# Performance work log

Measured on AMD Instinct MI355X. Metric: run time of the kernel, lower is better.

The kernel has to match this reference:

```python
import jax, jax.numpy as jnp
import numpy as np

EPS = 1e-6
N_HEADS = 16
D_HEAD = 64

def _rmsnorm(x, scale):
    rms = jnp.sqrt(jnp.mean(x * x, axis=-1, keepdims=True) + EPS)
    return x / rms * scale

def setup_inputs() -> dict:
    key = jax.random.key(0)
    ks = jax.random.split(key, 8)
    B, L, D = 512, 64, 1024
    return {
        "x": jax.random.normal(ks[0], (B, L, D), dtype=jnp.float32),
        "rel_indices": jax.random.randint(ks[1], (L, L), 0, 225, dtype=jnp.int64),
        "Wq": jax.random.normal(ks[2], (D, D), dtype=jnp.float32) * 0.02,
        "Wk": jax.random.normal(ks[3], (D, D), dtype=jnp.float32) * 0.02,
        "Wv": jax.random.normal(ks[4], (D, D), dtype=jnp.float32) * 0.02,
        "Wo": jax.random.normal(ks[5], (D, D), dtype=jnp.float32) * 0.02,
        "q_scale": jnp.ones((D_HEAD,), dtype=jnp.float32),
        "k_scale": jnp.ones((D_HEAD,), dtype=jnp.float32),
        "rel_k": jax.random.normal(ks[6], (225, D_HEAD), dtype=jnp.float32) * 0.02,
        "rel_v": jax.random.normal(ks[7], (225, D_HEAD), dtype=jnp.float32) * 0.02,
    }

def reference(x, rel_indices, Wq, Wk, Wv, Wo, q_scale, k_scale, rel_k, rel_v):
    B, L, D = x.shape
    H, dk = N_HEADS, D_HEAD
    scale = 1.0 / jnp.sqrt(jnp.float32(dk))
    # projections; Linear with weight W applied as x @ W (bias=False)
    q = (x @ Wq).reshape(B, L, H, dk)
    k = (x @ Wk).reshape(B, L, H, dk)
    v = (x @ Wv).reshape(B, L, H, dk).transpose(0, 2, 1, 3)  # bhld
    q = _rmsnorm(q, q_scale).transpose(0, 2, 1, 3)  # bhld
    k = _rmsnorm(k, k_scale).transpose(0, 2, 1, 3)  # bhld
    r_k = rel_k[rel_indices]  # [L, L, dk]
    r_v = rel_v[rel_indices]  # [L, L, dk]
    content = jnp.einsum('bhid,bhjd->bhij', q, k)
    rel = jnp.einsum('bhid,ijd->bhij', q, r_k)
    probs = jax.nn.softmax((content + rel) * scale, axis=-1)
    out = jnp.einsum('bhij,bhjd->bhid', probs, v) + jnp.einsum('bhij,ijd->bhid', probs, r_v)
    out = out.transpose(0, 2, 1, 3).reshape(B, L, D)
    return out @ Wo
```

## Files before the change

### kernel.cpp

```cpp
#include <hip/hip_runtime.h>
#include <stdint.h>

typedef unsigned short u16;
typedef __attribute__((ext_vector_type(8))) short s16x8;
typedef __attribute__((ext_vector_type(4))) float f32x4;

#define DEV static __device__ __forceinline__

#define MFMA16(a, b, c) __builtin_amdgcn_mfma_f32_16x16x32_bf16((a), (b), (c), 0, 0, 0)

DEV u16 f2b(float f) {
  unsigned u = __float_as_uint(f);
  unsigned r = (u + 0x7fffu + ((u >> 16) & 1u)) >> 16;
  return (u16)r;
}
DEV float b2f(u16 u) { return __uint_as_float(((unsigned)u) << 16); }

typedef const __attribute__((address_space(1))) unsigned int* as1p;
typedef __attribute__((address_space(3))) unsigned int* as3p;

DEV void gload16(const void* g, void* l) {
  __builtin_amdgcn_global_load_lds((as1p)(uintptr_t)g, (as3p)(unsigned)(uintptr_t)l, 16, 0, 0);
}

DEV void ldsPkAddBf16(void* ldsPtr, unsigned packed) {
  unsigned addr = (unsigned)(uintptr_t)ldsPtr;
  asm volatile("ds_pk_add_bf16 %0, %1" : : "v"(addr), "v"(packed) : "memory");
}

__global__ void conv_x_k(const float* __restrict__ x, u16* __restrict__ xb) {
  const int n8 = 32768 * 1024 / 8;
  int i = blockIdx.x * 256 + threadIdx.x;
  int stride = gridDim.x * 256;
  for (; i < n8; i += stride) {
    const float4* p = (const float4*)x + (size_t)i * 2;
    float4 a = p[0], c = p[1];
    union { s16x8 v; u16 u[8]; } o;
    o.u[0] = f2b(a.x); o.u[1] = f2b(a.y); o.u[2] = f2b(a.z); o.u[3] = f2b(a.w);
    o.u[4] = f2b(c.x); o.u[5] = f2b(c.y); o.u[6] = f2b(c.z); o.u[7] = f2b(c.w);
    *(s16x8*)(xb + (size_t)i * 8) = o.v;
  }
}

__global__ void transp_w_k(const float* __restrict__ Wq, const float* __restrict__ Wk,
                           const float* __restrict__ Wv, const float* __restrict__ Wo,
                           u16* __restrict__ wqkT, u16* __restrict__ wvT, u16* __restrict__ woT) {
  const int z = blockIdx.z;
  const float* src = z == 0 ? Wq : z == 1 ? Wk : z == 2 ? Wv : Wo;
  u16* dst = z == 0 ? wqkT : z == 1 ? (wqkT + 1024 * 1024) : z == 2 ? wvT : woT;
  __shared__ u16 t[64][72];
  const int kb = blockIdx.y * 64, nb = blockIdx.x * 64;
  const int tid = threadIdx.x;
  const int c = tid & 63, r0 = tid >> 6;
  #pragma unroll
  for (int s = 0; s < 16; ++s) {
    int r = r0 * 16 + s;
    t[r][c] = f2b(src[(size_t)(kb + r) * 1024 + nb + c]);
  }
  __syncthreads();
  #pragma unroll
  for (int s = 0; s < 16; ++s) {
    int n = r0 * 16 + s;
    dst[(size_t)(nb + n) * 1024 + kb + c] = t[c][n];
  }
}

__global__ void prep_rel_k(const float* __restrict__ rk, const float* __restrict__ rv,
                           u16* __restrict__ rkb, u16* __restrict__ rvT) {
  int i = blockIdx.x * 256 + threadIdx.x;
  if (i < 240 * 64) {
    int tt = i >> 6, d = i & 63;
    rkb[i] = (tt < 225) ? f2b(rk[tt * 64 + d]) : (u16)0;
  }
  if (i < 64 * 256) {
    int d = i >> 8, tt = i & 255;
    rvT[i] = (tt < 225) ? f2b(rv[tt * 64 + d]) : (u16)0;
  }
}

template <int EPI>
__global__ __launch_bounds__(256, 2)
void gemm_k(const u16* __restrict__ A, const u16* __restrict__ BT,
            u16* __restrict__ o16a, u16* __restrict__ o16b,
            float* __restrict__ oF,
            const float* __restrict__ qsc, const float* __restrict__ ksc) {
  __shared__ u16 smA[2][128 * 32];
  __shared__ u16 smB[2][128 * 32];
  const int tid = threadIdx.x;
  const int w = tid >> 6, l = tid & 63;
  const int lc = l & 15, l4 = l >> 4;
  const int nwg = gridDim.x * gridDim.y;
  const int orig = blockIdx.y * gridDim.x + blockIdx.x;
  const int wg = ((orig & 7) * (nwg >> 3)) + (orig >> 3);
  const int bx = wg % gridDim.x, by = wg / gridDim.x;
  const int m0 = by * 128, n0 = bx * 128;
  const int wm = (w >> 1) * 64, wn = (w & 1) * 64;

  f32x4 acc[4][4];
  #pragma unroll
  for (int i = 0; i < 4; ++i)
    #pragma unroll
    for (int j = 0; j < 4; ++j) acc[i][j] = (f32x4){0.f, 0.f, 0.f, 0.f};

  int srcRow[2], srcCol[2];
  #pragma unroll
  for (int s = 0; s < 2; ++s) {
    int p = w * 2048 + s * 1024 + l * 16;
    int row = p >> 6;
    int lb = p ^ (((row ^ (row >> 2)) & 3) << 4);
    srcRow[s] = row;
    srcCol[s] = (lb & 63) >> 1;
  }

  auto stage = [&](int buf, int kt) {
    #pragma unroll
    for (int s = 0; s < 2; ++s) {
      int base = w * 2048 + s * 1024;
      const u16* ga = A + (size_t)(m0 + srcRow[s]) * 1024 + kt * 32 + srcCol[s];
      gload16(ga, (char*)&smA[buf][0] + base);
      const u16* gb = BT + (size_t)(n0 + srcRow[s]) * 1024 + kt * 32 + srcCol[s];
      gload16(gb, (char*)&smB[buf][0] + base);
    }
  };
  auto fragA = [&](int buf, int mf) -> s16x8 {
    int row = wm + mf * 16 + lc;
    int p = (row << 6) + (l4 << 4);
    p ^= ((row ^ (row >> 2)) & 3) << 4;
    return *(const s16x8*)((const char*)&smA[buf][0] + p);
  };
  auto fragB = [&](int buf, int nf) -> s16x8 {
    int row = wn + nf * 16 + lc;
    int p = (row << 6) + (l4 << 4);
    p ^= ((row ^ (row >> 2)) & 3) << 4;
    return *(const s16x8*)((const char*)&smB[buf][0] + p);
  };

  stage(0, 0);
  __syncthreads();
  #pragma unroll 2
  for (int kt = 0; kt < 32; ++kt) {
    int cur = kt & 1;
    if (kt + 1 < 32) stage(cur ^ 1, kt + 1);
    s16x8 af[4], bf[4];
    #pragma unroll
    for (int i = 0; i < 4; ++i) { af[i] = fragA(cur, i); bf[i] = fragB(cur, i); }
    #pragma unroll
    for (int mf = 0; mf < 4; ++mf)
      #pragma unroll
      for (int nf = 0; nf < 4; ++nf)
        acc[mf][nf] = MFMA16(af[mf], bf[nf], acc[mf][nf]);
    __syncthreads();
  }

  if constexpr (EPI == 2) {
    #pragma unroll
    for (int mf = 0; mf < 4; ++mf)
      #pragma unroll
      for (int r = 0; r < 4; ++r) {
        int gm = m0 + wm + mf * 16 + l4 * 4 + r;
        #pragma unroll
        for (int nf = 0; nf < 4; ++nf) {
          int gn = n0 + wn + nf * 16 + lc;
          oF[(size_t)gm * 1024 + gn] = acc[mf][nf][r];
        }
      }
  } else if constexpr (EPI == 1) {
    #pragma unroll
    for (int mf = 0; mf < 4; ++mf)
      #pragma unroll
      for (int r = 0; r < 4; ++r) {
        int gm = m0 + wm + mf * 16 + l4 * 4 + r;
        #pragma unroll
        for (int nf = 0; nf < 4; ++nf) {
          int gn = n0 + wn + nf * 16 + lc;
          size_t addr = (((size_t)(gn >> 6) * 16 + (gm >> 6)) * 64 + (gm & 63)) * 64 + (gn & 63);
          o16a[addr] = f2b(acc[mf][nf][r]);
        }
      }
  } else {
    int nw0 = n0 + wn;
    bool isq = nw0 < 1024;
    const float* sc = isq ? qsc : ksc;
    u16* dst = isq ? o16a : o16b;
    int h = (nw0 & 1023) >> 6;
    float scv[4];
    #pragma unroll
    for (int nf = 0; nf < 4; ++nf) scv[nf] = sc[nf * 16 + lc];
    #pragma unroll
    for (int mf = 0; mf < 4; ++mf)
      #pragma unroll
      for (int r = 0; r < 4; ++r) {
        float ss = 0.f;
        #pragma unroll
        for (int nf = 0; nf < 4; ++nf) ss += acc[mf][nf][r] * acc[mf][nf][r];
        #pragma unroll
        for (int mask = 1; mask < 16; mask <<= 1) ss += __shfl_xor(ss, mask, 64);
        float rinv = rsqrtf(ss * 0.015625f + 1e-6f);
        int gm = m0 + wm + mf * 16 + l4 * 4 + r;
        size_t base = (((size_t)(gm >> 6) * 16 + h) * 64 + (gm & 63)) * 64;
        #pragma unroll
        for (int nf = 0; nf < 4; ++nf)
          dst[base + nf * 16 + lc] = f2b(acc[mf][nf][r] * rinv * scv[nf]);
      }
  }
}

DEV int rwByte(int row, int t) {
  return row * 512 + ((((t >> 3) ^ (row & 7)) << 4)) + ((t & 7) * 2);
}

__global__ __launch_bounds__(256, 3)
void attn_k(const u16* __restrict__ qn, const u16* __restrict__ kn,
            const u16* __restrict__ vT, const u16* __restrict__ rkb,
            const u16* __restrict__ rvT, const int* __restrict__ ridx,
            u16* __restrict__ ao) {
  __shared__ u16 RW[64 * 256];
  __shared__ u16 Pl[64 * 72];
  const int bid = blockIdx.x;
  const int b = bid >> 4, h = bid & 15;
  const int tid = threadIdx.x;
  const int w = tid >> 6, l = tid & 63;
  const int lc = l & 15, l4 = l >> 4;
  const int i0 = w * 16;
  const size_t hb = (size_t)(b * 16 + h) * 4096;
  const u16* qh = qn + hb;
  const u16* kh = kn + hb;
  const u16* vh = vT + hb;

  int ts[4][4];
  #pragma unroll
  for (int q = 0; q < 4; ++q) {
    int row = i0 + l4 * 4 + q;
    #pragma unroll
    for (int nf = 0; nf < 4; ++nf) ts[nf][q] = ridx[row * 64 + nf * 16 + lc];
  }
  s16x8 aq0 = *(const s16x8*)(qh + (i0 + lc) * 64 + l4 * 8);
  s16x8 aq1 = *(const s16x8*)(qh + (i0 + lc) * 64 + 32 + l4 * 8);
  s16x8 kb0[4], kb1[4], vb0[4], vb1[4];
  #pragma unroll
  for (int nf = 0; nf < 4; ++nf) {
    kb0[nf] = *(const s16x8*)(kh + (nf * 16 + lc) * 64 + l4 * 8);
    kb1[nf] = *(const s16x8*)(kh + (nf * 16 + lc) * 64 + 32 + l4 * 8);
    vb0[nf] = *(const s16x8*)(vh + (nf * 16 + lc) * 64 + l4 * 8);
    vb1[nf] = *(const s16x8*)(vh + (nf * 16 + lc) * 64 + 32 + l4 * 8);
  }

  f32x4 accC[4];
  #pragma unroll
  for (int nf = 0; nf < 4; ++nf) accC[nf] = (f32x4){0.f, 0.f, 0.f, 0.f};
  #pragma unroll
  for (int nf = 0; nf < 4; ++nf) {
    accC[nf] = MFMA16(aq0, kb0[nf], accC[nf]);
    accC[nf] = MFMA16(aq1, kb1[nf], accC[nf]);
  }

  #pragma unroll
  for (int c = 0; c < 3; ++c) {
    s16x8 rb0[5], rb1[5];
    #pragma unroll
    for (int u = 0; u < 5; ++u) {
      int t0 = (c * 5 + u) * 16;
      rb0[u] = *(const s16x8*)(rkb + (t0 + lc) * 64 + l4 * 8);
      rb1[u] = *(const s16x8*)(rkb + (t0 + lc) * 64 + 32 + l4 * 8);
    }
    #pragma unroll
    for (int u = 0; u < 5; ++u) {
      f32x4 rr = (f32x4){0.f, 0.f, 0.f, 0.f};
      rr = MFMA16(aq0, rb0[u], rr);
      rr = MFMA16(aq1, rb1[u], rr);
      int t = (c * 5 + u) * 16 + lc;
      #pragma unroll
      for (int q = 0; q < 4; ++q) {
        int row = i0 + l4 * 4 + q;
        RW[rwByte(row, t) >> 1] = f2b(rr[q]);
      }
    }
  }
  __syncthreads();

  float ev[4][4];
  float linv[4];
  #pragma unroll
  for (int q = 0; q < 4; ++q) {
    int row = i0 + l4 * 4 + q;
    float mx = -1e30f;
    #pragma unroll
    for (int nf = 0; nf < 4; ++nf) {
      float r = b2f(RW[rwByte(row, ts[nf][q]) >> 1]);
      float s = (accC[nf][q] + r) * 0.125f;
      ev[nf][q] = s;
      mx = fmaxf(mx, s);
    }
    #pragma unroll
    for (int mask = 1; mask < 16; mask <<= 1) mx = fmaxf(mx, __shfl_xor(mx, mask, 64));
    float sum = 0.f;
    #pragma unroll
    for (int nf = 0; nf < 4; ++nf) { float e = __expf(ev[nf][q] - mx); ev[nf][q] = e; sum += e; }
    #pragma unroll
    for (int mask = 1; mask < 16; mask <<= 1) sum += __shfl_xor(sum, mask, 64);
    linv[q] = 1.f / sum;
    #pragma unroll
    for (int nf = 0; nf < 4; ++nf) Pl[row * 72 + nf * 16 + lc] = f2b(ev[nf][q]);
  }
  __syncthreads();

  f32x4 accO[4];
  #pragma unroll
  for (int nf = 0; nf < 4; ++nf) accO[nf] = (f32x4){0.f, 0.f, 0.f, 0.f};
  s16x8 pa0 = *(const s16x8*)(&Pl[(i0 + lc) * 72 + l4 * 8]);
  s16x8 pa1 = *(const s16x8*)(&Pl[(i0 + lc) * 72 + 32 + l4 * 8]);
  {
    s16x8 z;
    #pragma unroll
    for (int j = 0; j < 8; ++j) z[j] = 0;
    #pragma unroll
    for (int zz = 0; zz < 8; ++zz) ((s16x8*)RW)[zz * 256 + tid] = z;
  }
  #pragma unroll
  for (int nf = 0; nf < 4; ++nf) {
    accO[nf] = MFMA16(pa0, vb0[nf], accO[nf]);
    accO[nf] = MFMA16(pa1, vb1[nf], accO[nf]);
  }
  __syncthreads();

  #pragma unroll
  for (int q = 0; q < 4; ++q)
    #pragma unroll
    for (int nf = 0; nf < 4; ++nf) {
      int row = i0 + l4 * 4 + q;
      int t = ts[nf][q];
      int byte = row * 512 + ((((t >> 3) ^ (row & 7)) << 4)) + ((t & 6) * 2);
      unsigned pk = ((unsigned)f2b(ev[nf][q])) << ((t & 1) * 16);
      ldsPkAddBf16((char*)RW + byte, pk);
    }
  asm volatile("s_waitcnt lgkmcnt(0)" ::: "memory");
  __syncthreads();

  #pragma unroll
  for (int kc = 0; kc < 4; ++kc) {
    s16x8 rb[2][4], wa[2];
    #pragma unroll
    for (int s = 0; s < 2; ++s) {
      int ks = kc * 2 + s;
      int row = i0 + lc;
      wa[s] = *(const s16x8*)((const char*)RW + row * 512 + ((((ks * 4 + l4) ^ (row & 7))) << 4));
      #pragma unroll
      for (int nf = 0; nf < 4; ++nf)
        rb[s][nf] = *(const s16x8*)(rvT + (nf * 16 + lc) * 256 + ks * 32 + l4 * 8);
    }
    #pragma unroll
    for (int s = 0; s < 2; ++s)
      #pragma unroll
      for (int nf = 0; nf < 4; ++nf)
        accO[nf] = MFMA16(wa[s], rb[s][nf], accO[nf]);
  }

  #pragma unroll
  for (int q = 0; q < 4; ++q) {
    int row = i0 + l4 * 4 + q;
    #pragma unroll
    for (int nf = 0; nf < 4; ++nf) {
      int d = nf * 16 + lc;
      ao[((size_t)(b * 64 + row)) * 1024 + h * 64 + d] = f2b(accO[nf][q] * linv[q]);
    }
  }
}

extern "C" void kernel_launch(void* const* d_in, const int* in_sizes, int n_in,
                              void* d_out, int out_size, void* d_ws, size_t ws_size,
                              hipStream_t stream) {
  (void)in_sizes; (void)n_in; (void)out_size; (void)ws_size;
  const float* x  = (const float*)d_in[0];
  const int* ridx = (const int*)d_in[1];
  const float* Wq = (const float*)d_in[2];
  const float* Wk = (const float*)d_in[3];
  const float* Wv = (const float*)d_in[4];
  const float* Wo = (const float*)d_in[5];
  const float* qs = (const float*)d_in[6];
  const float* ks = (const float*)d_in[7];
  const float* rk = (const float*)d_in[8];
  const float* rv = (const float*)d_in[9];
  float* out = (float*)d_out;

  char* ws = (char*)d_ws;
  const size_t SZ = 32768ull * 1024 * 2;
  u16* xb   = (u16*)(ws);
  u16* qn   = (u16*)(ws + SZ);
  u16* kn   = (u16*)(ws + 2 * SZ);
  u16* vT   = (u16*)(ws + 3 * SZ);
  u16* wqkT = (u16*)(ws + 4 * SZ);
  u16* wvT  = (u16*)(ws + 4 * SZ + 4194304);
  u16* woT  = (u16*)(ws + 4 * SZ + 6291456);
  u16* rkb  = (u16*)(ws + 4 * SZ + 8388608);
  u16* rvTb = (u16*)(ws + 4 * SZ + 8388608 + 30720);

  conv_x_k<<<2048, 256, 0, stream>>>(x, xb);
  transp_w_k<<<dim3(16, 16, 4), 256, 0, stream>>>(Wq, Wk, Wv, Wo, wqkT, wvT, woT);
  prep_rel_k<<<64, 256, 0, stream>>>(rk, rv, rkb, rvTb);
  gemm_k<0><<<dim3(16, 256), 256, 0, stream>>>(xb, wqkT, qn, kn, nullptr, qs, ks);
  gemm_k<1><<<dim3(256, 8), 256, 0, stream>>>(wvT, xb, vT, nullptr, nullptr, nullptr, nullptr);
  attn_k<<<8192, 256, 0, stream>>>(qn, kn, vT, rkb, rvTb, ridx, xb);
  gemm_k<2><<<dim3(8, 256), 256, 0, stream>>>(xb, woT, nullptr, nullptr, out, nullptr, nullptr);
}
```

Before: 966.0 us.

## Stage K/V in swizzled LDS via async loads and batch rel table prefetch

K and V tiles for each head are now copied into XOR-swizzled shared memory with global_load_lds, so each wave reads its fragments from LDS instead of every wave fetching all of K and V from global memory. All 15 rel_k tiles are loaded up front, and all rel_v fragments are loaded before the probability-weighted accumulation, which hides more memory latency. The cost is much higher register use and more LDS, so launch bounds drop from 3 to 2 blocks per CU and occupancy may fall.

```diff
diff --git a/kernel.cpp b/kernel.cpp
--- a/kernel.cpp
+++ b/kernel.cpp
@@ -209,11 +209,13 @@
   return row * 512 + ((((t >> 3) ^ (row & 7)) << 4)) + ((t & 7) * 2);
 }
 
-__global__ __launch_bounds__(256, 3)
+__global__ __launch_bounds__(256, 2)
 void attn_k(const u16* __restrict__ qn, const u16* __restrict__ kn,
             const u16* __restrict__ vT, const u16* __restrict__ rkb,
             const u16* __restrict__ rvT, const int* __restrict__ ridx,
             u16* __restrict__ ao) {
+  __shared__ u16 Ksm[64 * 64];
+  __shared__ u16 Vsm[64 * 64];
   __shared__ u16 RW[64 * 256];
   __shared__ u16 Pl[64 * 72];
   const int bid = blockIdx.x;
@@ -227,6 +229,16 @@
   const u16* kh = kn + hb;
   const u16* vh = vT + hb;
 
+  #pragma unroll
+  for (int s = 0; s < 2; ++s) {
+    int p = w * 2048 + s * 1024 + l * 16;
+    int t = p >> 7;
+    int sl = ((p >> 4) & 7) ^ (t & 7);
+    int e = t * 64 + sl * 8;
+    gload16(kh + e, (char*)Ksm + w * 2048 + s * 1024);
+    gload16(vh + e, (char*)Vsm + w * 2048 + s * 1024);
+  }
+
   int ts[4][4];
   #pragma unroll
   for (int q = 0; q < 4; ++q) {
@@ -236,39 +248,35 @@
   }
   s16x8 aq0 = *(const s16x8*)(qh + (i0 + lc) * 64 + l4 * 8);
   s16x8 aq1 = *(const s16x8*)(qh + (i0 + lc) * 64 + 32 + l4 * 8);
-  s16x8 kb0[4], kb1[4], vb0[4], vb1[4];
-  #pragma unroll
-  for (int nf = 0; nf < 4; ++nf) {
-    kb0[nf] = *(const s16x8*)(kh + (nf * 16 + lc) * 64 + l4 * 8);
-    kb1[nf] = *(const s16x8*)(kh + (nf * 16 + lc) * 64 + 32 + l4 * 8);
-    vb0[nf] = *(const s16x8*)(vh + (nf * 16 + lc) * 64 + l4 * 8);
-    vb1[nf] = *(const s16x8*)(vh + (nf * 16 + lc) * 64 + 32 + l4 * 8);
-  }
 
   f32x4 accC[4];
   #pragma unroll
   for (int nf = 0; nf < 4; ++nf) accC[nf] = (f32x4){0.f, 0.f, 0.f, 0.f};
-  #pragma unroll
-  for (int nf = 0; nf < 4; ++nf) {
-    accC[nf] = MFMA16(aq0, kb0[nf], accC[nf]);
-    accC[nf] = MFMA16(aq1, kb1[nf], accC[nf]);
-  }
-
-  #pragma unroll
-  for (int c = 0; c < 3; ++c) {
-    s16x8 rb0[5], rb1[5];
-    #pragma unroll
-    for (int u = 0; u < 5; ++u) {
-      int t0 = (c * 5 + u) * 16;
-      rb0[u] = *(const s16x8*)(rkb + (t0 + lc) * 64 + l4 * 8);
-      rb1[u] = *(const s16x8*)(rkb + (t0 + lc) * 64 + 32 + l4 * 8);
-    }
-    #pragma unroll
-    for (int u = 0; u < 5; ++u) {
+
+  {
+    s16x8 rb0[15], rb1[15];
+    #pragma unroll
+    for (int u = 0; u < 15; ++u) {
+      rb0[u] = *(const s16x8*)(rkb + (u * 16 + lc) * 64 + l4 * 8);
+      rb1[u] = *(const s16x8*)(rkb + (u * 16 + lc) * 64 + 32 + l4 * 8);
+    }
+    __syncthreads();
+
+    #pragma unroll
+    for (int nf = 0; nf < 4; ++nf) {
+      int row = nf * 16 + lc;
+      s16x8 k0 = *(const s16x8*)((const char*)Ksm + row * 128 + (((0 + l4) ^ (row & 7)) << 4));
+      s16x8 k1 = *(const s16x8*)((const char*)Ksm + row * 128 + (((4 + l4) ^ (row & 7)) << 4));
+      accC[nf] = MFMA16(aq0, k0, accC[nf]);
+      accC[nf] = MFMA16(aq1, k1, accC[nf]);
+    }
+
+    #pragma unroll
+    for (int u = 0; u < 15; ++u) {
       f32x4 rr = (f32x4){0.f, 0.f, 0.f, 0.f};
       rr = MFMA16(aq0, rb0[u], rr);
       rr = MFMA16(aq1, rb1[u], rr);
-      int t = (c * 5 + u) * 16 + lc;
+      int t = u * 16 + lc;
       #pragma unroll
       for (int q = 0; q < 4; ++q) {
         int row = i0 + l4 * 4 + q;
@@ -304,22 +312,31 @@
   }
   __syncthreads();
 
+  s16x8 rvf[8][4];
+  #pragma unroll
+  for (int ks = 0; ks < 8; ++ks)
+    #pragma unroll
+    for (int nf = 0; nf < 4; ++nf)
+      rvf[ks][nf] = *(const s16x8*)(rvT + (nf * 16 + lc) * 256 + ks * 32 + l4 * 8);
+  {
+    s16x8 z;
+    #pragma unroll
+    for (int j = 0; j < 8; ++j) z[j] = 0;
+    #pragma unroll
+    for (int zz = 0; zz < 8; ++zz) ((s16x8*)RW)[zz * 256 + tid] = z;
+  }
   f32x4 accO[4];
   #pragma unroll
   for (int nf = 0; nf < 4; ++nf) accO[nf] = (f32x4){0.f, 0.f, 0.f, 0.f};
   s16x8 pa0 = *(const s16x8*)(&Pl[(i0 + lc) * 72 + l4 * 8]);
   s16x8 pa1 = *(const s16x8*)(&Pl[(i0 + lc) * 72 + 32 + l4 * 8]);
-  {
-    s16x8 z;
-    #pragma unroll
-    for (int j = 0; j < 8; ++j) z[j] = 0;
-    #pragma unroll
-    for (int zz = 0; zz < 8; ++zz) ((s16x8*)RW)[zz * 256 + tid] = z;
-  }
   #pragma unroll
   for (int nf = 0; nf < 4; ++nf) {
-    accO[nf] = MFMA16(pa0, vb0[nf], accO[nf]);
-    accO[nf] = MFMA16(pa1, vb1[nf], accO[nf]);
+    int row = nf * 16 + lc;
+    s16x8 v0 = *(const s16x8*)((const char*)Vsm + row * 128 + (((0 + l4) ^ (row & 7)) << 4));
+    s16x8 v1 = *(const s16x8*)((const char*)Vsm + row * 128 + (((4 + l4) ^ (row & 7)) << 4));
+    accO[nf] = MFMA16(pa0, v0, accO[nf]);
+    accO[nf] = MFMA16(pa1, v1, accO[nf]);
   }
   __syncthreads();
 
@@ -337,22 +354,12 @@
   __syncthreads();
 
   #pragma unroll
-  for (int kc = 0; kc < 4; ++kc) {
-    s16x8 rb[2][4], wa[2];
-    #pragma unroll
-    for (int s = 0; s < 2; ++s) {
-      int ks = kc * 2 + s;
-      int row = i0 + lc;
-      wa[s] = *(const s16x8*)((const char*)RW + row * 512 + ((((ks * 4 + l4) ^ (row & 7))) << 4));
-      #pragma unroll
-      for (int nf = 0; nf < 4; ++nf)
-        rb[s][nf] = *(const s16x8*)(rvT + (nf * 16 + lc) * 256 + ks * 32 + l4 * 8);
-    }
-    #pragma unroll
-    for (int s = 0; s < 2; ++s)
-      #pragma unroll
-      for (int nf = 0; nf < 4; ++nf)
-        accO[nf] = MFMA16(wa[s], rb[s][nf], accO[nf]);
+  for (int ks = 0; ks < 8; ++ks) {
+    int row = i0 + lc;
+    s16x8 wa = *(const s16x8*)((const char*)RW + row * 512 + ((((ks * 4 + l4) ^ (row & 7))) << 4));
+    #pragma unroll
+    for (int nf = 0; nf < 4; ++nf)
+      accO[nf] = MFMA16(wa, rvf[ks][nf], accO[nf]);
   }
 
   #pragma unroll
```

Result: no change. 955.6 us (-1.1%).
